# Performance work log

Measured on AMD Instinct MI355X. Metric: run time of the kernel, lower is better.

The kernel has to match this reference:

```python
import jax, jax.numpy as jnp
import numpy as np

H, E, V, B, S = 512, 256, 50000, 128, 200


def setup_inputs() -> dict:
    key = jax.random.key(0)
    ks = jax.random.split(key, 12)
    s = 0.02
    return {
        "x": jax.random.randint(ks[0], (B,), 0, V),
        "hidden": jax.random.normal(ks[1], (1, B, H), jnp.float32),
        "enc_out": jax.random.normal(ks[2], (B, S, 2 * H), jnp.float32),
        "emb": jax.random.normal(ks[3], (V, E), jnp.float32) * s,
        "attn_w": jax.random.normal(ks[4], (H, 3 * H), jnp.float32) * s,
        "attn_b": jnp.zeros((H,), jnp.float32),
        "v": jax.random.uniform(ks[5], (H,), jnp.float32),
        "w_ih": jax.random.normal(ks[6], (3 * H, 2 * H + E), jnp.float32) * s,
        "w_hh": jax.random.normal(ks[7], (3 * H, H), jnp.float32) * s,
        "b_ih": jnp.zeros((3 * H,), jnp.float32),
        "b_hh": jnp.zeros((3 * H,), jnp.float32),
        "out_w": jax.random.normal(ks[8], (V, 3 * H + E), jnp.float32) * s,
        "out_b": jnp.zeros((V,), jnp.float32),
    }


def _gru_cell(x, h, w_ih, w_hh, b_ih, b_hh):
    # PyTorch GRU gate order: r, z, n
    gi = x @ w_ih.T + b_ih          # [B, 3H]
    gh = h @ w_hh.T + b_hh          # [B, 3H]
    i_r, i_z, i_n = jnp.split(gi, 3, axis=-1)
    h_r, h_z, h_n = jnp.split(gh, 3, axis=-1)
    r = jax.nn.sigmoid(i_r + h_r)
    z = jax.nn.sigmoid(i_z + h_z)
    n = jnp.tanh(i_n + r * h_n)
    return (1.0 - z) * n + z * h


def reference(x, hidden, enc_out, emb, attn_w, attn_b, v, w_ih, w_hh, b_ih, b_hh, out_w, out_b):
    emb_x = emb[x]                                   # [B, E]
    h0 = hidden[0]                                   # [B, H]
    b, s, _ = enc_out.shape
    hid_rep = jnp.broadcast_to(h0[:, None, :], (b, s, h0.shape[-1]))
    concat = jnp.concatenate([hid_rep, enc_out], axis=2)      # [B, S, 3H]
    att_l1 = concat @ attn_w.T + attn_b                        # [B, S, H] (no activation, per source)
    scores = jnp.einsum("bsh,h->bs", att_l1, v)               # [B, S]
    attn = jax.nn.softmax(scores, axis=1)
    context = jnp.einsum("bs,bsd->bd", attn, enc_out)         # [B, 2H]
    to_gru = jax.nn.relu(jnp.concatenate([emb_x, context], axis=1))  # [B, E+2H]
    h_new = _gru_cell(to_gru, h0, w_ih, w_hh, b_ih, b_hh)     # [B, H]
    to_out = jnp.concatenate([h_new, context, emb_x], axis=1)  # [B, 3H+E]
    logits = to_out @ out_w.T + out_b                          # [B, V]
    return logits, h_new[None]
```

## Files before the change

kernel.cpp:

```cpp
#include <hip/hip_runtime.h>
#include <hip/hip_bf16.h>

#define BB 128
#define SS 200
#define HH 512
#define EE 256
#define VV 50000
#define KGRU 1280
#define KOUT 1792
#define N3H 1536

typedef __bf16 bf16x8 __attribute__((ext_vector_type(8)));
typedef __bf16 bf16x4 __attribute__((ext_vector_type(4)));
typedef float  f32x4  __attribute__((ext_vector_type(4)));

__global__ __launch_bounds__(256) void u2_kernel(const float* __restrict__ attn_w,
                                                 const float* __restrict__ v,
                                                 float* __restrict__ u2) {
    int j = blockIdx.x * 256 + threadIdx.x;
    float acc = 0.f;
    #pragma unroll 8
    for (int h = 0; h < HH; h++)
        acc += v[h] * attn_w[h * N3H + HH + j];
    u2[j] = acc;
}

__global__ __launch_bounds__(256) void embx_kernel(const int* __restrict__ x,
                                                   const float* __restrict__ emb,
                                                   __bf16* __restrict__ Agru,
                                                   __bf16* __restrict__ Aout) {
    int b = blockIdx.x, e = threadIdx.x;
    float val = emb[(size_t)x[b] * EE + e];
    Aout[(size_t)b * KOUT + 3 * HH + e] = (__bf16)val;
    Agru[(size_t)b * KGRU + e]          = (__bf16)fmaxf(val, 0.f);
}

__global__ __launch_bounds__(256) void h0cast_kernel(const float* __restrict__ h0,
                                                     __bf16* __restrict__ Ah0) {
    int i = blockIdx.x * 256 + threadIdx.x;
    Ah0[i] = (__bf16)h0[i];
}

__global__ __launch_bounds__(256) void attn_kernel(const float* __restrict__ enc,
                                                   const float* __restrict__ u2,
                                                   float* __restrict__ context,
                                                   __bf16* __restrict__ Agru,
                                                   __bf16* __restrict__ Aout) {
    __shared__ float u2s[2 * HH];
    __shared__ float sc[SS];
    __shared__ float red[8];
    const int b = blockIdx.x, tid = threadIdx.x;
    const int wave = tid >> 6, lane = tid & 63;

    ((float4*)u2s)[tid] = ((const float4*)u2)[tid];
    __syncthreads();

    const float* encb = enc + (size_t)b * SS * 2 * HH;
    for (int s = wave; s < SS; s += 4) {
        const float4* row = (const float4*)(encb + s * 2 * HH);
        float acc = 0.f;
        #pragma unroll
        for (int i = 0; i < 4; i++) {
            float4 e = row[lane + i * 64];
            float4 u = ((const float4*)u2s)[lane + i * 64];
            acc += e.x * u.x + e.y * u.y + e.z * u.z + e.w * u.w;
        }
        #pragma unroll
        for (int off = 32; off; off >>= 1) acc += __shfl_xor(acc, off);
        if (lane == 0) sc[s] = acc;
    }
    __syncthreads();

    float vv = (tid < SS) ? sc[tid] : -3.4e38f;
    float m = vv;
    #pragma unroll
    for (int off = 32; off; off >>= 1) m = fmaxf(m, __shfl_xor(m, off));
    if (lane == 0) red[wave] = m;
    __syncthreads();
    m = fmaxf(fmaxf(red[0], red[1]), fmaxf(red[2], red[3]));
    float p = (tid < SS) ? __expf(vv - m) : 0.f;
    float ssum = p;
    #pragma unroll
    for (int off = 32; off; off >>= 1) ssum += __shfl_xor(ssum, off);
    if (lane == 0) red[4 + wave] = ssum;
    __syncthreads();
    float tot = red[4] + red[5] + red[6] + red[7];
    if (tid < SS) sc[tid] = p / tot;
    __syncthreads();

    float accd[4] = {0.f, 0.f, 0.f, 0.f};
    for (int s = 0; s < SS; s++) {
        float ps = sc[s];
        const float* row = encb + s * 2 * HH;
        #pragma unroll
        for (int i = 0; i < 4; i++) accd[i] += ps * row[tid + i * 256];
    }
    #pragma unroll
    for (int i = 0; i < 4; i++) {
        int d = tid + i * 256;
        float c = accd[i];
        context[(size_t)b * 2 * HH + d] = c;
        Aout[(size_t)b * KOUT + HH + d] = (__bf16)c;
        Agru[(size_t)b * KGRU + EE + d] = (__bf16)fmaxf(c, 0.f);
    }
}

__global__ __launch_bounds__(256) void gemm_bf16(const __bf16* __restrict__ A,
                                                 const float* __restrict__ B,
                                                 const float* __restrict__ bias,
                                                 float* __restrict__ C,
                                                 int N, int K) {
    __shared__ __bf16 As[128][40];
    __shared__ __bf16 Bs[64][40];
    const int tid = threadIdx.x;
    const int wave = tid >> 6, lane = tid & 63;
    const int q = lane >> 4, r16 = lane & 15;
    const int n0 = blockIdx.x * 64;
    const int am = tid >> 1, ah = tid & 1;

    f32x4 acc[8];
    #pragma unroll
    for (int mt = 0; mt < 8; mt++) acc[mt] = f32x4{0.f, 0.f, 0.f, 0.f};

    for (int kc = 0; kc < K; kc += 32) {
        const uint4* ap = (const uint4*)(A + (size_t)am * K + kc + ah * 16);
        uint4 a0 = ap[0], a1 = ap[1];
        *(uint4*)(&As[am][ah * 16])     = a0;
        *(uint4*)(&As[am][ah * 16 + 8]) = a1;
        #pragma unroll
        for (int j = 0; j < 2; j++) {
            int idx = tid + j * 256;
            int row = idx >> 3, col = (idx & 7) * 4;
            float4 bv = make_float4(0.f, 0.f, 0.f, 0.f);
            if (n0 + row < N)
                bv = *(const float4*)(B + (size_t)(n0 + row) * K + kc + col);
            bf16x4 pk = { (__bf16)bv.x, (__bf16)bv.y, (__bf16)bv.z, (__bf16)bv.w };
            *(bf16x4*)(&Bs[row][col]) = pk;
        }
        __syncthreads();

        bf16x8 bfrag = *(const bf16x8*)(&Bs[wave * 16 + r16][q * 8]);
        #pragma unroll
        for (int mt = 0; mt < 8; mt++) {
            bf16x8 afrag = *(const bf16x8*)(&As[mt * 16 + r16][q * 8]);
            acc[mt] = __builtin_amdgcn_mfma_f32_16x16x32_bf16(afrag, bfrag, acc[mt], 0, 0, 0);
        }
        __syncthreads();
    }

    const int n = n0 + wave * 16 + r16;
    if (n < N) {
        float bv = bias[n];
        #pragma unroll
        for (int mt = 0; mt < 8; mt++)
            #pragma unroll
            for (int i = 0; i < 4; i++) {
                int mrow = mt * 16 + q * 4 + i;
                C[(size_t)mrow * N + n] = acc[mt][i] + bv;
            }
    }
}

__global__ __launch_bounds__(256) void gate_kernel(const float* __restrict__ gi,
                                                   const float* __restrict__ gh,
                                                   const float* __restrict__ h0,
                                                   float* __restrict__ hout,
                                                   __bf16* __restrict__ Aout) {
    int i = blockIdx.x * 256 + threadIdx.x;
    int b = i >> 9, h = i & 511;
    const float* gib = gi + (size_t)b * N3H;
    const float* ghb = gh + (size_t)b * N3H;
    float r = 1.f / (1.f + __expf(-(gib[h] + ghb[h])));
    float z = 1.f / (1.f + __expf(-(gib[HH + h] + ghb[HH + h])));
    float n = tanhf(gib[2 * HH + h] + r * ghb[2 * HH + h]);
    float hnew = (1.f - z) * n + z * h0[i];
    hout[i] = hnew;
    Aout[(size_t)b * KOUT + h] = (__bf16)hnew;
}

extern "C" void kernel_launch(void* const* d_in, const int* in_sizes, int n_in,
                              void* d_out, int out_size, void* d_ws, size_t ws_size,
                              hipStream_t stream) {
    const int*   x      = (const int*)  d_in[0];
    const float* hidden = (const float*)d_in[1];
    const float* enc    = (const float*)d_in[2];
    const float* emb    = (const float*)d_in[3];
    const float* attn_w = (const float*)d_in[4];
    const float* v      = (const float*)d_in[6];
    const float* w_ih   = (const float*)d_in[7];
    const float* w_hh   = (const float*)d_in[8];
    const float* b_ih   = (const float*)d_in[9];
    const float* b_hh   = (const float*)d_in[10];
    const float* out_w  = (const float*)d_in[11];
    const float* out_b  = (const float*)d_in[12];

    float* out = (float*)d_out;
    float* logits = out;
    float* hnew_out = out + (size_t)BB * VV;

    char* ws = (char*)d_ws;
    float*  u2      = (float*) (ws + 0);
    float*  context = (float*) (ws + 4096);
    float*  gi      = (float*) (ws + 528384);
    float*  gh      = (float*) (ws + 1314816);
    __bf16* Agru    = (__bf16*)(ws + 2101248);
    __bf16* Ah0     = (__bf16*)(ws + 2428928);
    __bf16* Aout    = (__bf16*)(ws + 2560000);

    u2_kernel<<<4, 256, 0, stream>>>(attn_w, v, u2);
    embx_kernel<<<BB, 256, 0, stream>>>(x, emb, Agru, Aout);
    h0cast_kernel<<<BB * HH / 256, 256, 0, stream>>>(hidden, Ah0);
    attn_kernel<<<BB, 256, 0, stream>>>(enc, u2, context, Agru, Aout);
    gemm_bf16<<<N3H / 64, 256, 0, stream>>>(Agru, w_ih, b_ih, gi, N3H, KGRU);
    gemm_bf16<<<N3H / 64, 256, 0, stream>>>(Ah0, w_hh, b_hh, gh, N3H, HH);
    gate_kernel<<<BB * HH / 256, 256, 0, stream>>>(gi, gh, hidden, hnew_out, Aout);
    gemm_bf16<<<(VV + 63) / 64, 256, 0, stream>>>(Aout, out_w, out_b, logits, VV, KOUT);
}
```

Before: 793.2 us.

## Split attention into parallel kernels, merge GRU GEMMs, widen output GEMM tile

The u2 reduction is now split across more blocks. The attention kernel is divided into a scores kernel (4 blocks per batch) and a context kernel (2 blocks per batch), so far more blocks run in parallel than the single block per batch used before. The embedding gather and h0 cast become one kernel, and the two GRU GEMMs become one launch. The output projection GEMM moves to 128-wide N tiles, which halves the A-tile reloads per output column and puts more MFMAs in each barrier interval, at the cost of more registers per thread.

```diff
diff --git a/kernel.cpp b/kernel.cpp
--- a/kernel.cpp
+++ b/kernel.cpp
@@ -17,46 +17,44 @@
 __global__ __launch_bounds__(256) void u2_kernel(const float* __restrict__ attn_w,
                                                  const float* __restrict__ v,
                                                  float* __restrict__ u2) {
-    int j = blockIdx.x * 256 + threadIdx.x;
+    __shared__ float part[4][64];
+    const int tid = threadIdx.x, wave = tid >> 6, lane = tid & 63;
+    const int j = blockIdx.x * 64 + lane;
+    const int h0 = wave * 128;
     float acc = 0.f;
     #pragma unroll 8
-    for (int h = 0; h < HH; h++)
-        acc += v[h] * attn_w[h * N3H + HH + j];
-    u2[j] = acc;
-}
-
-__global__ __launch_bounds__(256) void embx_kernel(const int* __restrict__ x,
+    for (int h = 0; h < 128; h++)
+        acc += v[h0 + h] * attn_w[(size_t)(h0 + h) * N3H + HH + j];
+    part[wave][lane] = acc;
+    __syncthreads();
+    if (wave == 0)
+        u2[j] = part[0][lane] + part[1][lane] + part[2][lane] + part[3][lane];
+}
+
+__global__ __launch_bounds__(256) void prep_kernel(const int* __restrict__ x,
                                                    const float* __restrict__ emb,
+                                                   const float* __restrict__ h0,
                                                    __bf16* __restrict__ Agru,
-                                                   __bf16* __restrict__ Aout) {
-    int b = blockIdx.x, e = threadIdx.x;
-    float val = emb[(size_t)x[b] * EE + e];
-    Aout[(size_t)b * KOUT + 3 * HH + e] = (__bf16)val;
-    Agru[(size_t)b * KGRU + e]          = (__bf16)fmaxf(val, 0.f);
-}
-
-__global__ __launch_bounds__(256) void h0cast_kernel(const float* __restrict__ h0,
-                                                     __bf16* __restrict__ Ah0) {
-    int i = blockIdx.x * 256 + threadIdx.x;
-    Ah0[i] = (__bf16)h0[i];
-}
-
-__global__ __launch_bounds__(256) void attn_kernel(const float* __restrict__ enc,
-                                                   const float* __restrict__ u2,
-                                                   float* __restrict__ context,
-                                                   __bf16* __restrict__ Agru,
-                                                   __bf16* __restrict__ Aout) {
+                                                   __bf16* __restrict__ Aout,
+                                                   __bf16* __restrict__ Ah0) {
+    const int b = blockIdx.x, t = threadIdx.x;
+    float val = emb[(size_t)x[b] * EE + t];
+    Aout[(size_t)b * KOUT + 3 * HH + t] = (__bf16)val;
+    Agru[(size_t)b * KGRU + t]          = (__bf16)fmaxf(val, 0.f);
+    Ah0[(size_t)b * HH + t]       = (__bf16)h0[(size_t)b * HH + t];
+    Ah0[(size_t)b * HH + t + 256] = (__bf16)h0[(size_t)b * HH + t + 256];
+}
+
+__global__ __launch_bounds__(256) void scores_kernel(const float* __restrict__ enc,
+                                                     const float* __restrict__ u2,
+                                                     float* __restrict__ scores) {
     __shared__ float u2s[2 * HH];
-    __shared__ float sc[SS];
-    __shared__ float red[8];
-    const int b = blockIdx.x, tid = threadIdx.x;
-    const int wave = tid >> 6, lane = tid & 63;
-
+    const int tid = threadIdx.x, wave = tid >> 6, lane = tid & 63;
+    const int b = blockIdx.x >> 2, s0 = (blockIdx.x & 3) * 50;
     ((float4*)u2s)[tid] = ((const float4*)u2)[tid];
     __syncthreads();
-
     const float* encb = enc + (size_t)b * SS * 2 * HH;
-    for (int s = wave; s < SS; s += 4) {
+    for (int s = s0 + wave; s < s0 + 50; s += 4) {
         const float4* row = (const float4*)(encb + s * 2 * HH);
         float acc = 0.f;
         #pragma unroll
@@ -67,11 +65,20 @@
         }
         #pragma unroll
         for (int off = 32; off; off >>= 1) acc += __shfl_xor(acc, off);
-        if (lane == 0) sc[s] = acc;
-    }
-    __syncthreads();
-
-    float vv = (tid < SS) ? sc[tid] : -3.4e38f;
+        if (lane == 0) scores[b * SS + s] = acc;
+    }
+}
+
+__global__ __launch_bounds__(256) void ctx_kernel(const float* __restrict__ enc,
+                                                  const float* __restrict__ scores,
+                                                  __bf16* __restrict__ Agru,
+                                                  __bf16* __restrict__ Aout) {
+    __shared__ float sc[SS];
+    __shared__ float red[8];
+    const int tid = threadIdx.x, wave = tid >> 6, lane = tid & 63;
+    const int b = blockIdx.x >> 1, d0 = (blockIdx.x & 1) * 512;
+
+    float vv = (tid < SS) ? scores[b * SS + tid] : -3.4e38f;
     float m = vv;
     #pragma unroll
     for (int off = 32; off; off >>= 1) m = fmaxf(m, __shfl_xor(m, off));
@@ -88,34 +95,44 @@
     if (tid < SS) sc[tid] = p / tot;
     __syncthreads();
 
-    float accd[4] = {0.f, 0.f, 0.f, 0.f};
-    for (int s = 0; s < SS; s++) {
-        float ps = sc[s];
-        const float* row = encb + s * 2 * HH;
-        #pragma unroll
-        for (int i = 0; i < 4; i++) accd[i] += ps * row[tid + i * 256];
-    }
-    #pragma unroll
-    for (int i = 0; i < 4; i++) {
-        int d = tid + i * 256;
-        float c = accd[i];
-        context[(size_t)b * 2 * HH + d] = c;
-        Aout[(size_t)b * KOUT + HH + d] = (__bf16)c;
-        Agru[(size_t)b * KGRU + EE + d] = (__bf16)fmaxf(c, 0.f);
-    }
-}
-
-__global__ __launch_bounds__(256) void gemm_bf16(const __bf16* __restrict__ A,
-                                                 const float* __restrict__ B,
-                                                 const float* __restrict__ bias,
-                                                 float* __restrict__ C,
-                                                 int N, int K) {
+    const float* encb = enc + (size_t)b * SS * 2 * HH + d0;
+    float a0 = 0.f, a1 = 0.f;
+    for (int s = 0; s < SS; s += 4) {
+        #pragma unroll
+        for (int k = 0; k < 4; k++) {
+            float ps = sc[s + k];
+            const float* row = encb + (s + k) * 2 * HH;
+            a0 += ps * row[tid];
+            a1 += ps * row[tid + 256];
+        }
+    }
+    int d = d0 + tid;
+    Aout[(size_t)b * KOUT + HH + d]       = (__bf16)a0;
+    Agru[(size_t)b * KGRU + EE + d]       = (__bf16)fmaxf(a0, 0.f);
+    Aout[(size_t)b * KOUT + HH + d + 256] = (__bf16)a1;
+    Agru[(size_t)b * KGRU + EE + d + 256] = (__bf16)fmaxf(a1, 0.f);
+}
+
+__global__ __launch_bounds__(256) void gru_gemms(const __bf16* __restrict__ Agru,
+                                                 const float* __restrict__ w_ih,
+                                                 const float* __restrict__ b_ih,
+                                                 float* __restrict__ gi,
+                                                 const __bf16* __restrict__ Ah0,
+                                                 const float* __restrict__ w_hh,
+                                                 const float* __restrict__ b_hh,
+                                                 float* __restrict__ gh) {
     __shared__ __bf16 As[128][40];
     __shared__ __bf16 Bs[64][40];
-    const int tid = threadIdx.x;
-    const int wave = tid >> 6, lane = tid & 63;
+    const bool second = blockIdx.x >= 24;
+    const __bf16* A   = second ? Ah0  : Agru;
+    const float*  B   = second ? w_hh : w_ih;
+    const float*  bias= second ? b_hh : b_ih;
+    float*        C   = second ? gh   : gi;
+    const int K = second ? HH : KGRU;
+    const int n0 = (blockIdx.x - (second ? 24 : 0)) * 64;
+
+    const int tid = threadIdx.x, wave = tid >> 6, lane = tid & 63;
     const int q = lane >> 4, r16 = lane & 15;
-    const int n0 = blockIdx.x * 64;
     const int am = tid >> 1, ah = tid & 1;
 
     f32x4 acc[8];
@@ -131,14 +148,11 @@
         for (int j = 0; j < 2; j++) {
             int idx = tid + j * 256;
             int row = idx >> 3, col = (idx & 7) * 4;
-            float4 bv = make_float4(0.f, 0.f, 0.f, 0.f);
-            if (n0 + row < N)
-                bv = *(const float4*)(B + (size_t)(n0 + row) * K + kc + col);
+            float4 bv = *(const float4*)(B + (size_t)(n0 + row) * K + kc + col);
             bf16x4 pk = { (__bf16)bv.x, (__bf16)bv.y, (__bf16)bv.z, (__bf16)bv.w };
             *(bf16x4*)(&Bs[row][col]) = pk;
         }
         __syncthreads();
-
         bf16x8 bfrag = *(const bf16x8*)(&Bs[wave * 16 + r16][q * 8]);
         #pragma unroll
         for (int mt = 0; mt < 8; mt++) {
@@ -147,18 +161,13 @@
         }
         __syncthreads();
     }
-
     const int n = n0 + wave * 16 + r16;
-    if (n < N) {
-        float bv = bias[n];
-        #pragma unroll
-        for (int mt = 0; mt < 8; mt++)
-            #pragma unroll
-            for (int i = 0; i < 4; i++) {
-                int mrow = mt * 16 + q * 4 + i;
-                C[(size_t)mrow * N + n] = acc[mt][i] + bv;
-            }
-    }
+    float bv = bias[n];
+    #pragma unroll
+    for (int mt = 0; mt < 8; mt++)
+        #pragma unroll
+        for (int i = 0; i < 4; i++)
+            C[(size_t)(mt * 16 + q * 4 + i) * N3H + n] = acc[mt][i] + bv;
 }
 
 __global__ __launch_bounds__(256) void gate_kernel(const float* __restrict__ gi,
@@ -178,6 +187,67 @@
     Aout[(size_t)b * KOUT + h] = (__bf16)hnew;
 }
 
+__global__ __launch_bounds__(256, 3) void gemm128(const __bf16* __restrict__ A,
+                                                  const float* __restrict__ B,
+                                                  const float* __restrict__ bias,
+                                                  float* __restrict__ C,
+                                                  int N, int K) {
+    __shared__ __bf16 As[128][40];
+    __shared__ __bf16 Bs[128][40];
+    const int tid = threadIdx.x, wave = tid >> 6, lane = tid & 63;
+    const int q = lane >> 4, r16 = lane & 15;
+    const int n0 = blockIdx.x * 128;
+    const int row = tid >> 1, half = tid & 1;
+
+    f32x4 acc[8][2];
+    #pragma unroll
+    for (int mt = 0; mt < 8; mt++) {
+        acc[mt][0] = f32x4{0.f, 0.f, 0.f, 0.f};
+        acc[mt][1] = f32x4{0.f, 0.f, 0.f, 0.f};
+    }
+
+    const bool brow_ok = (n0 + row) < N;
+    for (int kc = 0; kc < K; kc += 32) {
+        const uint4* ap = (const uint4*)(A + (size_t)row * K + kc + half * 16);
+        uint4 a0 = ap[0], a1 = ap[1];
+        float4 bv[4];
+        const float* bp = B + (size_t)(n0 + row) * K + kc + half * 16;
+        #pragma unroll
+        for (int i = 0; i < 4; i++)
+            bv[i] = brow_ok ? *(const float4*)(bp + i * 4) : make_float4(0.f, 0.f, 0.f, 0.f);
+        *(uint4*)(&As[row][half * 16])     = a0;
+        *(uint4*)(&As[row][half * 16 + 8]) = a1;
+        #pragma unroll
+        for (int i = 0; i < 4; i++) {
+            bf16x4 pk = { (__bf16)bv[i].x, (__bf16)bv[i].y, (__bf16)bv[i].z, (__bf16)bv[i].w };
+            *(bf16x4*)(&Bs[row][half * 16 + i * 4]) = pk;
+        }
+        __syncthreads();
+        bf16x8 bfrag0 = *(const bf16x8*)(&Bs[wave * 32 + r16][q * 8]);
+        bf16x8 bfrag1 = *(const bf16x8*)(&Bs[wave * 32 + 16 + r16][q * 8]);
+        #pragma unroll
+        for (int mt = 0; mt < 8; mt++) {
+            bf16x8 afrag = *(const bf16x8*)(&As[mt * 16 + r16][q * 8]);
+            acc[mt][0] = __builtin_amdgcn_mfma_f32_16x16x32_bf16(afrag, bfrag0, acc[mt][0], 0, 0, 0);
+            acc[mt][1] = __builtin_amdgcn_mfma_f32_16x16x32_bf16(afrag, bfrag1, acc[mt][1], 0, 0, 0);
+        }
+        __syncthreads();
+    }
+
+    #pragma unroll
+    for (int j = 0; j < 2; j++) {
+        int n = n0 + wave * 32 + j * 16 + r16;
+        if (n < N) {
+            float bvv = bias[n];
+            #pragma unroll
+            for (int mt = 0; mt < 8; mt++)
+                #pragma unroll
+                for (int i = 0; i < 4; i++)
+                    C[(size_t)(mt * 16 + q * 4 + i) * N + n] = acc[mt][j][i] + bvv;
+        }
+    }
+}
+
 extern "C" void kernel_launch(void* const* d_in, const int* in_sizes, int n_in,
                               void* d_out, int out_size, void* d_ws, size_t ws_size,
                               hipStream_t stream) {
@@ -200,19 +270,18 @@
 
     char* ws = (char*)d_ws;
     float*  u2      = (float*) (ws + 0);
-    float*  context = (float*) (ws + 4096);
-    float*  gi      = (float*) (ws + 528384);
-    float*  gh      = (float*) (ws + 1314816);
-    __bf16* Agru    = (__bf16*)(ws + 2101248);
-    __bf16* Ah0     = (__bf16*)(ws + 2428928);
-    __bf16* Aout    = (__bf16*)(ws + 2560000);
-
-    u2_kernel<<<4, 256, 0, stream>>>(attn_w, v, u2);
-    embx_kernel<<<BB, 256, 0, stream>>>(x, emb, Agru, Aout);
-    h0cast_kernel<<<BB * HH / 256, 256, 0, stream>>>(hidden, Ah0);
-    attn_kernel<<<BB, 256, 0, stream>>>(enc, u2, context, Agru, Aout);
-    gemm_bf16<<<N3H / 64, 256, 0, stream>>>(Agru, w_ih, b_ih, gi, N3H, KGRU);
-    gemm_bf16<<<N3H / 64, 256, 0, stream>>>(Ah0, w_hh, b_hh, gh, N3H, HH);
+    float*  scores  = (float*) (ws + 4096);
+    float*  gi      = (float*) (ws + 106496);
+    float*  gh      = (float*) (ws + 892928);
+    __bf16* Agru    = (__bf16*)(ws + 1679360);
+    __bf16* Ah0     = (__bf16*)(ws + 2007040);
+    __bf16* Aout    = (__bf16*)(ws + 2138112);
+
+    u2_kernel<<<16, 256, 0, stream>>>(attn_w, v, u2);
+    prep_kernel<<<BB, 256, 0, stream>>>(x, emb, hidden, Agru, Aout, Ah0);
+    scores_kernel<<<BB * 4, 256, 0, stream>>>(enc, u2, scores);
+    ctx_kernel<<<BB * 2, 256, 0, stream>>>(enc, scores, Agru, Aout);
+    gru_gemms<<<48, 256, 0, stream>>>(Agru, w_ih, b_ih, gi, Ah0, w_hh, b_hh, gh);
     gate_kernel<<<BB * HH / 256, 256, 0, stream>>>(gi, gh, hidden, hnew_out, Aout);
-    gemm_bf16<<<(VV + 63) / 64, 256, 0, stream>>>(Aout, out_w, out_b, logits, VV, KOUT);
-}
+    gemm128<<<(VV + 127) / 128, 256, 0, stream>>>(Aout, out_w, out_b, logits, VV, KOUT);
+}
```

New measurement: 699.1 us. 11.9% less time.
